# Kernel tuning notes

Measured on AMD Instinct MI355X. Metric: run time of the kernel, lower is better.

## Reference

```python
import jax, jax.numpy as jnp
from jax import lax
import numpy as np

H = 32  # hidden size
I = 1   # input size

def setup_inputs() -> dict:
    key = jax.random.key(0)
    ks = jax.random.split(key, 8)
    B, T = 4096, 512
    s_ih = 1.0 / np.sqrt(H)
    inp = {
        "x": jax.random.normal(ks[0], (B, T, I), dtype=jnp.float32),
        # PyTorch LSTM params, gate order (i, f, g, o)
        "W_ih": jax.random.uniform(ks[1], (4 * H, I), dtype=jnp.float32, minval=-s_ih, maxval=s_ih),
        "W_hh": jax.random.uniform(ks[2], (4 * H, H), dtype=jnp.float32, minval=-s_ih, maxval=s_ih),
        "b_ih": jax.random.uniform(ks[3], (4 * H,), dtype=jnp.float32, minval=-s_ih, maxval=s_ih),
        "b_hh": jax.random.uniform(ks[4], (4 * H,), dtype=jnp.float32, minval=-s_ih, maxval=s_ih),
        "W_head": jax.random.uniform(ks[5], (1, H), dtype=jnp.float32, minval=-s_ih, maxval=s_ih),
        "b_head": jax.random.uniform(ks[6], (1,), dtype=jnp.float32, minval=-s_ih, maxval=s_ih),
    }
    return inp

def reference(x, W_ih, W_hh, b_ih, b_hh, W_head, b_head):
    B, T, _ = x.shape
    # Precompute input contribution to all gates: [B, T, 4H]
    x_gates = jnp.einsum('bti,gi->btg', x, W_ih) + b_ih + b_hh

    def step(carry, xg_t):  # xg_t: [B, 4H]
        h, c = carry
        gates = xg_t + h @ W_hh.T
        i, f, g, o = jnp.split(gates, 4, axis=-1)
        i = jax.nn.sigmoid(i)
        f = jax.nn.sigmoid(f)
        g = jnp.tanh(g)
        o = jax.nn.sigmoid(o)
        c = f * c + i * g
        h = o * jnp.tanh(c)
        return (h, c), None

    h0 = jnp.zeros((B, H), dtype=x.dtype)
    c0 = jnp.zeros((B, H), dtype=x.dtype)
    (h_last, _), _ = lax.scan(step, (h0, c0), jnp.swapaxes(x_gates, 0, 1))
    # head on last timestep: [B, 1]
    return h_last @ W_head.T + b_head
```

## Files before the change

### kernel.cpp

```cpp
#include <hip/hip_runtime.h>

#define HID 32
#define SEQ 512
#define WAVES_PER_BLOCK 4
#define BLOCK (WAVES_PER_BLOCK * 64)

typedef float v2f __attribute__((ext_vector_type(2)));


#define PK2(WE, WO, R) \
  "v_pk_fma_f32 v[80:81], %[" WE "], " R ", v[80:81] op_sel_hi:[1,0,1]\n\t" \
  "v_pk_fma_f32 v[80:81], %[" WO "], " R ", v[80:81] op_sel:[0,1,0] op_sel_hi:[1,1,1]\n\t"

#define STEPSTR \
  "ds_read2_b32 v[82:83], v108 offset0:0 offset1:0\n\t" \
  "ds_read_b128 v[84:87], %[vRD] offset:0\n\t" \
  "ds_read_b128 v[88:91], %[vRD] offset:16\n\t" \
  "ds_read_b128 v[92:95], %[vRD] offset:32\n\t" \
  "ds_read_b128 v[96:99], %[vRD] offset:48\n\t" \
  "v_add_u32 v108, 4, v108\n\t" \
  "s_waitcnt lgkmcnt(4)\n\t" \
  "v_pk_fma_f32 v[80:81], %[uv], v[82:83], %[bv]\n\t" \
  "s_waitcnt lgkmcnt(3)\n\t" \
  PK2("w0","w1","v[84:85]") \
  PK2("w2","w3","v[86:87]") \
  "ds_read_b128 v[84:87], %[vRD] offset:64\n\t" \
  "s_waitcnt lgkmcnt(3)\n\t" \
  PK2("w4","w5","v[88:89]") \
  PK2("w6","w7","v[90:91]") \
  "ds_read_b128 v[88:91], %[vRD] offset:80\n\t" \
  "s_waitcnt lgkmcnt(3)\n\t" \
  PK2("w8","w9","v[92:93]") \
  PK2("w10","w11","v[94:95]") \
  "ds_read_b128 v[92:95], %[vRD] offset:96\n\t" \
  "s_waitcnt lgkmcnt(3)\n\t" \
  PK2("w12","w13","v[96:97]") \
  PK2("w14","w15","v[98:99]") \
  "ds_read_b128 v[96:99], %[vRD] offset:112\n\t" \
  "s_waitcnt lgkmcnt(3)\n\t" \
  PK2("w16","w17","v[84:85]") \
  PK2("w18","w19","v[86:87]") \
  "s_waitcnt lgkmcnt(2)\n\t" \
  PK2("w20","w21","v[88:89]") \
  PK2("w22","w23","v[90:91]") \
  "s_waitcnt lgkmcnt(1)\n\t" \
  PK2("w24","w25","v[92:93]") \
  PK2("w26","w27","v[94:95]") \
  "s_waitcnt lgkmcnt(0)\n\t" \
  PK2("w28","w29","v[96:97]") \
  PK2("w30","w31","v[98:99]") \
  "v_mul_f32 v100, %[vSX], v80\n\t" \
  "v_mul_f32 v103, 0xbfb8aa3b, v81\n\t" \
  "v_exp_f32 v100, v100\n\t" \
  "v_exp_f32 v103, v103\n\t" \
  "s_nop 1\n\t" \
  "v_add_f32 v100, 1.0, v100\n\t" \
  "v_add_f32 v103, 1.0, v103\n\t" \
  "v_rcp_f32 v101, v100\n\t" \
  "v_rcp_f32 v103, v103\n\t" \
  "s_nop 1\n\t" \
  "v_fma_f32 v102, %[vB], v101, %[vA]\n\t" \
  "ds_bpermute_b32 v104, %[vXOR], v102\n\t" \
  "ds_bpermute_b32 v105, %[vXOR], v103\n\t" \
  "s_waitcnt lgkmcnt(0)\n\t" \
  "v_mul_f32 v106, v102, v104\n\t" \
  "v_fma_f32 %[c], v103, %[c], v106\n\t" \
  "v_mul_f32 v107, 0x4038aa3b, %[c]\n\t" \
  "v_exp_f32 v107, v107\n\t" \
  "s_nop 1\n\t" \
  "v_add_f32 v107, 1.0, v107\n\t" \
  "v_rcp_f32 v107, v107\n\t" \
  "s_nop 1\n\t" \
  "v_fma_f32 v107, -2.0, v107, 1.0\n\t" \
  "v_mul_f32 %[h], v105, v107\n\t" \
  "ds_write_b32 %[vWR], %[h]\n\t"

#define S4  STEPSTR STEPSTR STEPSTR STEPSTR
#define X32 S4 S4 S4 S4 S4 S4 S4 S4

__global__ __launch_bounds__(BLOCK)
void lstm_fused_kernel(
    const float* __restrict__ x,
    const float* __restrict__ W_ih,
    const float* __restrict__ W_hh,
    const float* __restrict__ b_ih,
    const float* __restrict__ b_hh,
    const float* __restrict__ W_head,
    const float* __restrict__ b_head,
    float* __restrict__ out)
{
    __shared__ v2f WL[32 * 64];
    __shared__ __align__(64) float Hbuf[WAVES_PER_BLOCK][128];

    const int tid = threadIdx.x;
    for (int idx = tid; idx < 32 * 64; idx += BLOCK) {
        const int j    = idx >> 6;
        const int l    = idx & 63;
        const int rowA = ((l >> 5) << 6) + (l & 31);
        WL[idx] = (v2f){ W_hh[rowA * 32 + j], W_hh[(rowA + 32) * 32 + j] };
    }
    __syncthreads();

    const int  lane = tid & 63;
    const int  k    = lane & 31;
    const bool hi   = lane >= 32;
    const int  wid  = tid >> 6;
    const int  b    = blockIdx.x * WAVES_PER_BLOCK + wid;

    v2f w[HID];
#pragma unroll
    for (int j = 0; j < HID; ++j) w[j] = WL[j * 64 + lane];

    const int gA = (hi ? 64 : 0) + k;
    const int gB = gA + 32;
    const v2f bv = { b_ih[gA] + b_hh[gA], b_ih[gB] + b_hh[gB] };
    const v2f uv = { W_ih[gA], W_ih[gB] };

    float* Hrow = &Hbuf[wid][0];
    const unsigned vRD  = (unsigned)(size_t)Hrow;
    const unsigned vWR  = vRD + (hi ? 256u : 0u) + (unsigned)(k * 4);
    const unsigned vXOR = (unsigned)(((lane ^ 32) & 63) * 4);
    const float vSX = hi ?  2.8853900817779268f : -1.4426950408889634f;
    const float vA  = hi ?  1.0f :  0.0f;
    const float vB  = hi ? -2.0f :  1.0f;

    const float* xb = x + (size_t)b * SEQ;

    Hrow[k] = 0.0f;
    float h = 0.0f, c = 0.0f;

#pragma unroll 1
    for (int t0 = 0; t0 < SEQ; t0 += 32) {
        Hrow[32 + k] = xb[t0 + k];
        asm volatile(
            "v_add_u32 v108, 128, %[vRD]\n\t"
            X32
            : [h]"+v"(h), [c]"+v"(c)
            : [w0]"v"(w[0]),  [w1]"v"(w[1]),  [w2]"v"(w[2]),  [w3]"v"(w[3]),
              [w4]"v"(w[4]),  [w5]"v"(w[5]),  [w6]"v"(w[6]),  [w7]"v"(w[7]),
              [w8]"v"(w[8]),  [w9]"v"(w[9]),  [w10]"v"(w[10]),[w11]"v"(w[11]),
              [w12]"v"(w[12]),[w13]"v"(w[13]),[w14]"v"(w[14]),[w15]"v"(w[15]),
              [w16]"v"(w[16]),[w17]"v"(w[17]),[w18]"v"(w[18]),[w19]"v"(w[19]),
              [w20]"v"(w[20]),[w21]"v"(w[21]),[w22]"v"(w[22]),[w23]"v"(w[23]),
              [w24]"v"(w[24]),[w25]"v"(w[25]),[w26]"v"(w[26]),[w27]"v"(w[27]),
              [w28]"v"(w[28]),[w29]"v"(w[29]),[w30]"v"(w[30]),[w31]"v"(w[31]),
              [uv]"v"(uv), [bv]"v"(bv),
              [vRD]"v"(vRD), [vWR]"v"(vWR), [vXOR]"v"(vXOR),
              [vSX]"v"(vSX), [vA]"v"(vA), [vB]"v"(vB)
            : "memory",
              "v80","v81","v82","v83","v84","v85","v86","v87","v88","v89",
              "v90","v91","v92","v93","v94","v95","v96","v97","v98","v99",
              "v100","v101","v102","v103","v104","v105","v106","v107","v108");
    }

    const float hf = Hrow[k];
    float v = hf * W_head[k];
#pragma unroll
    for (int off = 16; off >= 1; off >>= 1)
        v += __shfl_xor(v, off, 32);
    if (lane == 0) out[b] = v + b_head[0];
}

extern "C" void kernel_launch(void* const* d_in, const int* in_sizes, int n_in,
                              void* d_out, int out_size, void* d_ws, size_t ws_size,
                              hipStream_t stream) {
    const float* x      = (const float*)d_in[0];
    const float* W_ih   = (const float*)d_in[1];
    const float* W_hh   = (const float*)d_in[2];
    const float* b_ih   = (const float*)d_in[3];
    const float* b_hh   = (const float*)d_in[4];
    const float* W_head = (const float*)d_in[5];
    const float* b_head = (const float*)d_in[6];
    float* out = (float*)d_out;

    const int B = in_sizes[0] / SEQ;
    const int grid = B / WAVES_PER_BLOCK;

    lstm_fused_kernel<<<grid, BLOCK, 0, stream>>>(
        x, W_ih, W_hh, b_ih, b_hh, W_head, b_head, out);
}
```

Before: 341.9 us.

## Broadcast hidden state via v_readlane into SGPRs instead of LDS round-trip

Each step now broadcasts the 32 hidden values and the current input with v_readlane into scalar registers. The packed FMAs read those scalars directly, which removes the per-step ds_write, the ds_read_b128 sequence, the lgkmcnt waits and the LDS staging buffer. The cost is 33 serialized readlane instructions per timestep plus possible VALU-to-SGPR read hazards. The final head now uses the in-register h instead of reading it back from LDS.

```diff
diff --git a/kernel.cpp b/kernel.cpp
--- a/kernel.cpp
+++ b/kernel.cpp
@@ -8,75 +8,75 @@
 typedef float v2f __attribute__((ext_vector_type(2)));
 
 
-#define PK2(WE, WO, R) \
-  "v_pk_fma_f32 v[80:81], %[" WE "], " R ", v[80:81] op_sel_hi:[1,0,1]\n\t" \
-  "v_pk_fma_f32 v[80:81], %[" WO "], " R ", v[80:81] op_sel:[0,1,0] op_sel_hi:[1,1,1]\n\t"
+#define PKS(WE, WO, SP) \
+  "v_pk_fma_f32 v[80:81], %[" WE "], s[" SP "], v[80:81] op_sel_hi:[1,0,1]\n\t" \
+  "v_pk_fma_f32 v[80:81], %[" WO "], s[" SP "], v[80:81] op_sel:[0,1,0] op_sel_hi:[1,1,1]\n\t"
 
-#define STEPSTR \
-  "ds_read2_b32 v[82:83], v108 offset0:0 offset1:0\n\t" \
-  "ds_read_b128 v[84:87], %[vRD] offset:0\n\t" \
-  "ds_read_b128 v[88:91], %[vRD] offset:16\n\t" \
-  "ds_read_b128 v[92:95], %[vRD] offset:32\n\t" \
-  "ds_read_b128 v[96:99], %[vRD] offset:48\n\t" \
-  "v_add_u32 v108, 4, v108\n\t" \
-  "s_waitcnt lgkmcnt(4)\n\t" \
-  "v_pk_fma_f32 v[80:81], %[uv], v[82:83], %[bv]\n\t" \
-  "s_waitcnt lgkmcnt(3)\n\t" \
-  PK2("w0","w1","v[84:85]") \
-  PK2("w2","w3","v[86:87]") \
-  "ds_read_b128 v[84:87], %[vRD] offset:64\n\t" \
-  "s_waitcnt lgkmcnt(3)\n\t" \
-  PK2("w4","w5","v[88:89]") \
-  PK2("w6","w7","v[90:91]") \
-  "ds_read_b128 v[88:91], %[vRD] offset:80\n\t" \
-  "s_waitcnt lgkmcnt(3)\n\t" \
-  PK2("w8","w9","v[92:93]") \
-  PK2("w10","w11","v[94:95]") \
-  "ds_read_b128 v[92:95], %[vRD] offset:96\n\t" \
-  "s_waitcnt lgkmcnt(3)\n\t" \
-  PK2("w12","w13","v[96:97]") \
-  PK2("w14","w15","v[98:99]") \
-  "ds_read_b128 v[96:99], %[vRD] offset:112\n\t" \
-  "s_waitcnt lgkmcnt(3)\n\t" \
-  PK2("w16","w17","v[84:85]") \
-  PK2("w18","w19","v[86:87]") \
-  "s_waitcnt lgkmcnt(2)\n\t" \
-  PK2("w20","w21","v[88:89]") \
-  PK2("w22","w23","v[90:91]") \
-  "s_waitcnt lgkmcnt(1)\n\t" \
-  PK2("w24","w25","v[92:93]") \
-  PK2("w26","w27","v[94:95]") \
+#define RLH \
+  "v_readlane_b32 s40, %[h], 0\n\t"  "v_readlane_b32 s41, %[h], 1\n\t" \
+  "v_readlane_b32 s42, %[h], 2\n\t"  "v_readlane_b32 s43, %[h], 3\n\t" \
+  "v_readlane_b32 s44, %[h], 4\n\t"  "v_readlane_b32 s45, %[h], 5\n\t" \
+  "v_readlane_b32 s46, %[h], 6\n\t"  "v_readlane_b32 s47, %[h], 7\n\t" \
+  "v_readlane_b32 s48, %[h], 8\n\t"  "v_readlane_b32 s49, %[h], 9\n\t" \
+  "v_readlane_b32 s50, %[h], 10\n\t" "v_readlane_b32 s51, %[h], 11\n\t" \
+  "v_readlane_b32 s52, %[h], 12\n\t" "v_readlane_b32 s53, %[h], 13\n\t" \
+  "v_readlane_b32 s54, %[h], 14\n\t" "v_readlane_b32 s55, %[h], 15\n\t" \
+  "v_readlane_b32 s56, %[h], 16\n\t" "v_readlane_b32 s57, %[h], 17\n\t" \
+  "v_readlane_b32 s58, %[h], 18\n\t" "v_readlane_b32 s59, %[h], 19\n\t" \
+  "v_readlane_b32 s60, %[h], 20\n\t" "v_readlane_b32 s61, %[h], 21\n\t" \
+  "v_readlane_b32 s62, %[h], 22\n\t" "v_readlane_b32 s63, %[h], 23\n\t" \
+  "v_readlane_b32 s64, %[h], 24\n\t" "v_readlane_b32 s65, %[h], 25\n\t" \
+  "v_readlane_b32 s66, %[h], 26\n\t" "v_readlane_b32 s67, %[h], 27\n\t" \
+  "v_readlane_b32 s68, %[h], 28\n\t" "v_readlane_b32 s69, %[h], 29\n\t" \
+  "v_readlane_b32 s70, %[h], 30\n\t" "v_readlane_b32 s71, %[h], 31\n\t"
+
+#define STEPSTR(TT) \
+  "s_nop 0\n\t" \
+  "v_readlane_b32 s38, %[xv], " TT "\n\t" \
+  RLH \
+  "v_pk_fma_f32 v[80:81], %[uv], s[38:39], %[bv] op_sel_hi:[1,0,1]\n\t" \
+  PKS("w0","w1","40:41")   PKS("w2","w3","42:43") \
+  PKS("w4","w5","44:45")   PKS("w6","w7","46:47") \
+  PKS("w8","w9","48:49")   PKS("w10","w11","50:51") \
+  PKS("w12","w13","52:53") PKS("w14","w15","54:55") \
+  PKS("w16","w17","56:57") PKS("w18","w19","58:59") \
+  PKS("w20","w21","60:61") PKS("w22","w23","62:63") \
+  PKS("w24","w25","64:65") PKS("w26","w27","66:67") \
+  PKS("w28","w29","68:69") PKS("w30","w31","70:71") \
+  "v_mul_f32 v84, %[vSX], v80\n\t" \
+  "v_mul_f32 v85, 0xbfb8aa3b, v81\n\t" \
+  "v_exp_f32 v84, v84\n\t" \
+  "v_exp_f32 v85, v85\n\t" \
+  "s_nop 1\n\t" \
+  "v_add_f32 v84, 1.0, v84\n\t" \
+  "v_add_f32 v85, 1.0, v85\n\t" \
+  "v_rcp_f32 v84, v84\n\t" \
+  "v_rcp_f32 v85, v85\n\t" \
+  "s_nop 1\n\t" \
+  "v_fma_f32 v86, %[vB], v84, %[vA]\n\t" \
+  "ds_bpermute_b32 v87, %[vXOR], v86\n\t" \
+  "ds_bpermute_b32 v88, %[vXOR], v85\n\t" \
   "s_waitcnt lgkmcnt(0)\n\t" \
-  PK2("w28","w29","v[96:97]") \
-  PK2("w30","w31","v[98:99]") \
-  "v_mul_f32 v100, %[vSX], v80\n\t" \
-  "v_mul_f32 v103, 0xbfb8aa3b, v81\n\t" \
-  "v_exp_f32 v100, v100\n\t" \
-  "v_exp_f32 v103, v103\n\t" \
+  "v_mul_f32 v89, v86, v87\n\t" \
+  "v_fma_f32 %[c], v85, %[c], v89\n\t" \
+  "v_mul_f32 v90, 0x4038aa3b, %[c]\n\t" \
+  "v_exp_f32 v90, v90\n\t" \
   "s_nop 1\n\t" \
-  "v_add_f32 v100, 1.0, v100\n\t" \
-  "v_add_f32 v103, 1.0, v103\n\t" \
-  "v_rcp_f32 v101, v100\n\t" \
-  "v_rcp_f32 v103, v103\n\t" \
+  "v_add_f32 v90, 1.0, v90\n\t" \
+  "v_rcp_f32 v90, v90\n\t" \
   "s_nop 1\n\t" \
-  "v_fma_f32 v102, %[vB], v101, %[vA]\n\t" \
-  "ds_bpermute_b32 v104, %[vXOR], v102\n\t" \
-  "ds_bpermute_b32 v105, %[vXOR], v103\n\t" \
-  "s_waitcnt lgkmcnt(0)\n\t" \
-  "v_mul_f32 v106, v102, v104\n\t" \
-  "v_fma_f32 %[c], v103, %[c], v106\n\t" \
-  "v_mul_f32 v107, 0x4038aa3b, %[c]\n\t" \
-  "v_exp_f32 v107, v107\n\t" \
-  "s_nop 1\n\t" \
-  "v_add_f32 v107, 1.0, v107\n\t" \
-  "v_rcp_f32 v107, v107\n\t" \
-  "s_nop 1\n\t" \
-  "v_fma_f32 v107, -2.0, v107, 1.0\n\t" \
-  "v_mul_f32 %[h], v105, v107\n\t" \
-  "ds_write_b32 %[vWR], %[h]\n\t"
+  "v_fma_f32 v90, -2.0, v90, 1.0\n\t" \
+  "v_mul_f32 %[h], v88, v90\n\t"
 
-#define S4  STEPSTR STEPSTR STEPSTR STEPSTR
-#define X32 S4 S4 S4 S4 S4 S4 S4 S4
+#define X32 \
+  STEPSTR("0")  STEPSTR("1")  STEPSTR("2")  STEPSTR("3") \
+  STEPSTR("4")  STEPSTR("5")  STEPSTR("6")  STEPSTR("7") \
+  STEPSTR("8")  STEPSTR("9")  STEPSTR("10") STEPSTR("11") \
+  STEPSTR("12") STEPSTR("13") STEPSTR("14") STEPSTR("15") \
+  STEPSTR("16") STEPSTR("17") STEPSTR("18") STEPSTR("19") \
+  STEPSTR("20") STEPSTR("21") STEPSTR("22") STEPSTR("23") \
+  STEPSTR("24") STEPSTR("25") STEPSTR("26") STEPSTR("27") \
+  STEPSTR("28") STEPSTR("29") STEPSTR("30") STEPSTR("31")
 
 __global__ __launch_bounds__(BLOCK)
 void lstm_fused_kernel(
@@ -90,7 +90,6 @@
     float* __restrict__ out)
 {
     __shared__ v2f WL[32 * 64];
-    __shared__ __align__(64) float Hbuf[WAVES_PER_BLOCK][128];
 
     const int tid = threadIdx.x;
     for (int idx = tid; idx < 32 * 64; idx += BLOCK) {
@@ -116,9 +115,6 @@
     const v2f bv = { b_ih[gA] + b_hh[gA], b_ih[gB] + b_hh[gB] };
     const v2f uv = { W_ih[gA], W_ih[gB] };
 
-    float* Hrow = &Hbuf[wid][0];
-    const unsigned vRD  = (unsigned)(size_t)Hrow;
-    const unsigned vWR  = vRD + (hi ? 256u : 0u) + (unsigned)(k * 4);
     const unsigned vXOR = (unsigned)(((lane ^ 32) & 63) * 4);
     const float vSX = hi ?  2.8853900817779268f : -1.4426950408889634f;
     const float vA  = hi ?  1.0f :  0.0f;
@@ -126,14 +122,12 @@
 
     const float* xb = x + (size_t)b * SEQ;
 
-    Hrow[k] = 0.0f;
     float h = 0.0f, c = 0.0f;
 
 #pragma unroll 1
     for (int t0 = 0; t0 < SEQ; t0 += 32) {
-        Hrow[32 + k] = xb[t0 + k];
+        const float xv = xb[t0 + k];
         asm volatile(
-            "v_add_u32 v108, 128, %[vRD]\n\t"
             X32
             : [h]"+v"(h), [c]"+v"(c)
             : [w0]"v"(w[0]),  [w1]"v"(w[1]),  [w2]"v"(w[2]),  [w3]"v"(w[3]),
@@ -144,17 +138,16 @@
               [w20]"v"(w[20]),[w21]"v"(w[21]),[w22]"v"(w[22]),[w23]"v"(w[23]),
               [w24]"v"(w[24]),[w25]"v"(w[25]),[w26]"v"(w[26]),[w27]"v"(w[27]),
               [w28]"v"(w[28]),[w29]"v"(w[29]),[w30]"v"(w[30]),[w31]"v"(w[31]),
-              [uv]"v"(uv), [bv]"v"(bv),
-              [vRD]"v"(vRD), [vWR]"v"(vWR), [vXOR]"v"(vXOR),
+              [uv]"v"(uv), [bv]"v"(bv), [xv]"v"(xv), [vXOR]"v"(vXOR),
               [vSX]"v"(vSX), [vA]"v"(vA), [vB]"v"(vB)
-            : "memory",
-              "v80","v81","v82","v83","v84","v85","v86","v87","v88","v89",
-              "v90","v91","v92","v93","v94","v95","v96","v97","v98","v99",
-              "v100","v101","v102","v103","v104","v105","v106","v107","v108");
+            : "v80","v81","v84","v85","v86","v87","v88","v89","v90",
+              "s38","s40","s41","s42","s43","s44","s45","s46","s47",
+              "s48","s49","s50","s51","s52","s53","s54","s55","s56","s57",
+              "s58","s59","s60","s61","s62","s63","s64","s65","s66","s67",
+              "s68","s69","s70","s71");
     }
 
-    const float hf = Hrow[k];
-    float v = hf * W_head[k];
+    float v = h * W_head[k];
 #pragma unroll
     for (int off = 16; off >= 1; off >>= 1)
         v += __shfl_xor(v, off, 32);
```

After: 412.7 us. 1.21x slower.
